# Optimization experiments

Measured on AMD Instinct MI355X. Metric: run time of the kernel, lower is better.

The kernel has to match this reference:

```python
import jax, jax.numpy as jnp
import numpy as np

NUM_HEADS = 8
MAX_REL = 32  # max_relative_positions
LN_EPS = 1e-5


def _conv1x1(x, W, b):
    # x: (B, C, H, W), W: (Cout, Cin), b: (Cout,)
    return jnp.einsum('bchw,oc->bohw', x, W) + b[None, :, None, None]


def setup_inputs() -> dict:
    key = jax.random.key(0)
    ks = jax.random.split(key, 10)
    B, C, H, W = 2, 512, 48, 48
    L = H * W
    s = 1.0 / np.sqrt(C)
    inp = {
        'x': jax.random.normal(ks[0], (B, C, H, W), jnp.float32),
        'mask': jax.random.randint(ks[1], (1, NUM_HEADS, L, L), 0, 2).astype(bool),
        'learnable_pos': jax.random.normal(ks[2], (1, C, H, W), jnp.float32) * 0.02,
        'Wq': jax.random.normal(ks[3], (C, C), jnp.float32) * s,
        'bq': jnp.zeros((C,), jnp.float32),
        'Wk': jax.random.normal(ks[4], (C, C), jnp.float32) * s,
        'bk': jnp.zeros((C,), jnp.float32),
        'Wv': jax.random.normal(ks[5], (C, C), jnp.float32) * s,
        'bv': jnp.zeros((C,), jnp.float32),
        'Wo': jax.random.normal(ks[6], (C, C), jnp.float32) * s,
        'bo': jnp.zeros((C,), jnp.float32),
        'rel_table': jax.random.normal(ks[7], (NUM_HEADS, 2 * MAX_REL + 1), jnp.float32) * 0.02,
        'ln_gamma': jnp.ones((C,), jnp.float32),
        'ln_beta': jnp.zeros((C,), jnp.float32),
    }
    return inp


def reference(x, mask, learnable_pos, Wq, bq, Wk, bk, Wv, bv, Wo, bo,
              rel_table, ln_gamma, ln_beta):
    B, C, H, W = x.shape
    L = H * W
    hd = C // NUM_HEADS
    residual = x

    xp = x + learnable_pos
    q = _conv1x1(xp, Wq, bq)
    k = _conv1x1(xp, Wk, bk)
    v = _conv1x1(xp, Wv, bv)

    def split_heads(t):  # (B,C,H,W) -> (B, heads, L, hd)
        return t.reshape(B, NUM_HEADS, hd, L).transpose(0, 1, 3, 2)

    q, k, v = split_heads(q), split_heads(k), split_heads(v)

    scale = 1.0 / np.sqrt(hd).astype(np.float32)
    scores = jnp.einsum('bhld,bhmd->bhlm', q, k) * scale  # (B,H,L,L)

    # relative positional bias per head
    pos = jnp.arange(L)
    rp = jnp.clip(pos[:, None] - pos[None, :], -MAX_REL, MAX_REL) + MAX_REL  # (L,L)
    scores = scores + rel_table[:, rp][None]  # (1,heads,L,L) broadcast

    scores = jnp.where(mask, scores, jnp.float32(-1e9))
    attn = jax.nn.softmax(scores, axis=-1)

    out = jnp.einsum('bhlm,bhmd->bhld', attn, v)  # (B,heads,L,hd)
    out = out.transpose(0, 1, 3, 2).reshape(B, C, H, W)
    out = _conv1x1(out, Wo, bo)

    y = residual + out
    # LayerNorm over channels (channels-last permute in original)
    yl = y.transpose(0, 2, 3, 1)  # (B,H,W,C)
    mu = jnp.mean(yl, axis=-1, keepdims=True)
    var = jnp.var(yl, axis=-1, keepdims=True)
    yl = (yl - mu) * jax.lax.rsqrt(var + LN_EPS) * ln_gamma + ln_beta
    return yl.transpose(0, 3, 1, 2)
```

## Files before the change

kernel.cpp:

```cpp
#include <hip/hip_runtime.h>
#include <cstdint>

#define L_SEQ 2304
#define CDIM  512
#define NHEADS 8
#define HD    64
#define LL    ((size_t)L_SEQ * L_SEQ)
#define ROWS_TOT (16 * L_SEQ)
#define PERBL ((size_t)2 * L_SEQ * 512)

typedef short  s8v  __attribute__((ext_vector_type(8)));
typedef float  f4v  __attribute__((ext_vector_type(4)));

__device__ __forceinline__ ushort f2bf(float f) {
    union { float f; uint32_t u; } v; v.f = f;
    uint32_t u = v.u;
    uint32_t r = (u + 0x7FFFu + ((u >> 16) & 1u)) >> 16;
    return (ushort)r;
}

__device__ __forceinline__ float bf2f(ushort u) {
    union { uint32_t u; float f; } v; v.u = (uint32_t)u << 16;
    return v.f;
}

__global__ __launch_bounds__(256) void prep(
    const float* __restrict__ Wq, const float* __restrict__ Wk,
    const float* __restrict__ Wv, const float* __restrict__ Wo,
    const float* __restrict__ x, const float* __restrict__ pos,
    ushort* __restrict__ wf, ushort* __restrict__ xt)
{
    __shared__ ushort T[64][72];
    const int bx = blockIdx.x;
    const int t  = threadIdx.x;
    if (bx < 512) {
        const int i    = bx * 256 + t;
        const int lane = i & 63;
        const int F    = (i >> 6) & 63;
        const int ob   = (i >> 12) & 7;
        const int mat  = i >> 15;
        const float* src = (mat == 0) ? Wq : (mat == 1) ? Wk : (mat == 2) ? Wv : Wo;
        const int row = ob * 64 + (F & 3) * 16 + (lane & 15);
        const int col = (F >> 2) * 32 + (lane >> 4) * 8;
        const float4 w0 = *(const float4*)&src[(size_t)row * 512 + col];
        const float4 w1 = *(const float4*)&src[(size_t)row * 512 + col + 4];
        ushort4 o0, o1;
        o0.x = f2bf(w0.x); o0.y = f2bf(w0.y); o0.z = f2bf(w0.z); o0.w = f2bf(w0.w);
        o1.x = f2bf(w1.x); o1.y = f2bf(w1.y); o1.z = f2bf(w1.z); o1.w = f2bf(w1.w);
        *(ushort4*)&wf[(size_t)i * 8]     = o0;
        *(ushort4*)&wf[(size_t)i * 8 + 4] = o1;
    } else {
        const int bb = bx - 512;
        const int l0 = (bb % 36) * 64;
        const int c0 = ((bb / 36) & 7) * 64;
        const int b  = bb / 288;
        const int cc = t >> 2;
        const int l4 = (t & 3) * 16;
        const size_t off  = ((size_t)b * CDIM + c0 + cc) * L_SEQ + l0 + l4;
        const size_t poff = (size_t)(c0 + cc) * L_SEQ + l0 + l4;
        #pragma unroll
        for (int j4 = 0; j4 < 4; j4++) {
            const float4 xv = *(const float4*)&x[off + j4 * 4];
            const float4 pv = *(const float4*)&pos[poff + j4 * 4];
            T[cc][l4 + j4 * 4 + 0] = f2bf(xv.x + pv.x);
            T[cc][l4 + j4 * 4 + 1] = f2bf(xv.y + pv.y);
            T[cc][l4 + j4 * 4 + 2] = f2bf(xv.z + pv.z);
            T[cc][l4 + j4 * 4 + 3] = f2bf(xv.w + pv.w);
        }
        __syncthreads();
        const int lr = t >> 2;
        const int c4 = (t & 3) * 16;
        ushort o[16];
        #pragma unroll
        for (int j = 0; j < 16; j++) o[j] = T[c4 + j][lr];
        ushort* dst = &xt[((size_t)b * L_SEQ + l0 + lr) * 512 + c0 + c4];
        *(ushort4*)&dst[0]  = *(ushort4*)&o[0];
        *(ushort4*)&dst[4]  = *(ushort4*)&o[4];
        *(ushort4*)&dst[8]  = *(ushort4*)&o[8];
        *(ushort4*)&dst[12] = *(ushort4*)&o[12];
    }
}

__global__ __launch_bounds__(256) void qkv_mfma(
    const ushort* __restrict__ xt, const ushort* __restrict__ wf,
    const float* __restrict__ bq, const float* __restrict__ bk,
    const float* __restrict__ bv,
    ushort* __restrict__ q_t, ushort* __restrict__ k_t, ushort* __restrict__ v_t)
{
    const int l0 = blockIdx.x * 64;
    const int ob = blockIdx.y;
    const int o0 = ob * 64;
    const int b  = blockIdx.z;
    const int t = threadIdx.x, w = t >> 6, lane = t & 63;
    const int n16 = lane & 15, q4 = lane >> 4;

    const ushort* A = xt + ((size_t)b * L_SEQ + l0 + w * 16 + n16) * 512 + q4 * 8;

    s8v areg[16];
    #pragma unroll
    for (int i = 0; i < 16; i++) areg[i] = *(const s8v*)&A[i * 32];

    const size_t lb = (size_t)lane * 8;

    f4v acc[3][4] = {};
    for (int ks = 0; ks < 16; ks++) {
        s8v bf[3][4];
        #pragma unroll
        for (int m = 0; m < 3; m++)
            #pragma unroll
            for (int t4 = 0; t4 < 4; t4++)
                bf[m][t4] = *(const s8v*)&wf[
                    ((size_t)((m * 8 + ob) * 64 + ks * 4 + t4)) * 512 + lb];
        const s8v a = areg[ks];
        #pragma unroll
        for (int m = 0; m < 3; m++)
            #pragma unroll
            for (int t4 = 0; t4 < 4; t4++)
                acc[m][t4] = __builtin_amdgcn_mfma_f32_16x16x32_bf16(a, bf[m][t4], acc[m][t4], 0, 0, 0);
    }

    const int h = ob;
    const int rowbase = l0 + w * 16 + q4 * 4;

    #pragma unroll
    for (int m = 0; m < 2; m++) {
        const float* bias = (m == 0) ? bq : bk;
        const float sc = (m == 0) ? 0.125f : 1.0f;
        ushort* op = (m == 0 ? q_t : k_t) + ((size_t)(b * NHEADS + h)) * L_SEQ * HD;
        #pragma unroll
        for (int t4 = 0; t4 < 4; t4++) {
            const float bi = bias[o0 + t4 * 16 + n16];
            #pragma unroll
            for (int r = 0; r < 4; r++)
                op[(size_t)(rowbase + r) * HD + t4 * 16 + n16] = f2bf((acc[m][t4][r] + bi) * sc);
        }
    }
    {
        ushort* op = v_t + ((size_t)(b * NHEADS + h)) * HD * L_SEQ;
        #pragma unroll
        for (int t4 = 0; t4 < 4; t4++) {
            const float bi = bv[o0 + t4 * 16 + n16];
            ushort4 st;
            st.x = f2bf(acc[2][t4][0] + bi);
            st.y = f2bf(acc[2][t4][1] + bi);
            st.z = f2bf(acc[2][t4][2] + bi);
            st.w = f2bf(acc[2][t4][3] + bi);
            *(ushort4*)&op[(size_t)(t4 * 16 + n16) * L_SEQ + rowbase] = st;
        }
    }
}

__global__ __launch_bounds__(256) void flash_attn_mfma(
    const ushort* __restrict__ q, const ushort* __restrict__ k,
    const ushort* __restrict__ vt, const int* __restrict__ mask,
    const float* __restrict__ rel_table, ushort* __restrict__ Opart,
    float* __restrict__ Lpart)
{
    __shared__ __align__(16) ushort Kf[2][512 * 8];
    __shared__ __align__(16) ushort Vf[2][512 * 8];
    __shared__ __align__(16) ushort Pb[4 * 16 * 72];
    __shared__ float rt[65];

    const int t    = threadIdx.x;
    const int id   = blockIdx.x;
    const int h    = id & 7;
    const int s2   = id >> 3;
    const int b    = s2 & 1;
    const int half = (s2 >> 1) & 1;
    const int qb   = s2 >> 2;
    const int bh   = b * NHEADS + h;
    const int l0   = qb * 64;
    const int w    = t >> 6;
    const int lane = t & 63;
    const int n16  = lane & 15;
    const int q4   = lane >> 4;

    if (t < 65) rt[t] = rel_table[h * 65 + t];

    const ushort* qp = q  + (size_t)bh * L_SEQ * HD;
    const ushort* kp = k  + (size_t)bh * L_SEQ * HD;
    const ushort* vp = vt + (size_t)bh * HD * L_SEQ;
    const int*    mp = mask + (size_t)h * LL;

    const int qrow = l0 + w * 16 + n16;
    const s8v qA0 = *(const s8v*)&qp[(size_t)qrow * HD + q4 * 8];
    const s8v qA1 = *(const s8v*)&qp[(size_t)qrow * HD + 32 + q4 * 8];

    f4v O[4] = {{0.f,0.f,0.f,0.f},{0.f,0.f,0.f,0.f},{0.f,0.f,0.f,0.f},{0.f,0.f,0.f,0.f}};
    float lrun[4] = {0.f, 0.f, 0.f, 0.f};

    int sKey[2], sD0[2], sDd[2];
    #pragma unroll
    for (int cc = 0; cc < 2; cc++) {
        const int c = t + cc * 256;
        const int g = c >> 6;
        const int sT = g >> 1, sS = g & 1;
        const int sQ = (c >> 4) & 3, sN = c & 15;
        sKey[cc] = sT * 16 + sN;
        sD0[cc]  = sS * 32 + sQ * 8;
        sDd[cc]  = sT * 16 + sN;
    }

    const int rowbase = l0 + w * 16 + q4 * 4;
    const int kbase = half * 1152;

    s8v kreg[2], vreg[2];
    int mreg[4][4];
    #pragma unroll
    for (int cc = 0; cc < 2; cc++) {
        kreg[cc] = *(const s8v*)&kp[(size_t)(kbase + sKey[cc]) * HD + sD0[cc]];
        vreg[cc] = *(const s8v*)&vp[(size_t)sDd[cc] * L_SEQ + kbase + sD0[cc]];
    }
    #pragma unroll
    for (int t4 = 0; t4 < 4; t4++)
        #pragma unroll
        for (int r = 0; r < 4; r++)
            mreg[t4][r] = mp[(size_t)(rowbase + r) * L_SEQ + kbase + t4 * 16 + n16];

    int par = 0;
    for (int mt = 0; mt < 18; mt++) {
        const int mb = kbase + mt * 64;
        ushort* Kb = &Kf[par][0];
        ushort* Vb = &Vf[par][0];
        #pragma unroll
        for (int cc = 0; cc < 2; cc++) {
            const int c = t + cc * 256;
            *(s8v*)&Kb[c * 8] = kreg[cc];
            *(s8v*)&Vb[c * 8] = vreg[cc];
        }
        __syncthreads();

        const int mb2 = (mt < 17) ? mb + 64 : mb;
        s8v knx[2], vnx[2];
        int mnx[4][4];
        #pragma unroll
        for (int cc = 0; cc < 2; cc++) {
            knx[cc] = *(const s8v*)&kp[(size_t)(mb2 + sKey[cc]) * HD + sD0[cc]];
            vnx[cc] = *(const s8v*)&vp[(size_t)sDd[cc] * L_SEQ + mb2 + sD0[cc]];
        }
        #pragma unroll
        for (int t4 = 0; t4 < 4; t4++)
            #pragma unroll
            for (int r = 0; r < 4; r++)
                mnx[t4][r] = mp[(size_t)(rowbase + r) * L_SEQ + mb2 + t4 * 16 + n16];

        f4v S[4];
        #pragma unroll
        for (int t4 = 0; t4 < 4; t4++) {
            const s8v b0 = *(const s8v*)&Kb[((t4 * 2 + 0) * 64 + lane) * 8];
            const s8v b1 = *(const s8v*)&Kb[((t4 * 2 + 1) * 64 + lane) * 8];
            f4v acc = {0.f, 0.f, 0.f, 0.f};
            acc = __builtin_amdgcn_mfma_f32_16x16x32_bf16(qA0, b0, acc, 0, 0, 0);
            acc = __builtin_amdgcn_mfma_f32_16x16x32_bf16(qA1, b1, acc, 0, 0, 0);
            S[t4] = acc;
        }

        #pragma unroll
        for (int t4 = 0; t4 < 4; t4++) {
            const int A = (l0 + w * 16) - (mb + t4 * 16);
            if (A >= 47) {
                const float bu = rt[64];
                #pragma unroll
                for (int r = 0; r < 4; r++) S[t4][r] += bu;
            } else if (A <= -47) {
                const float bu = rt[0];
                #pragma unroll
                for (int r = 0; r < 4; r++) S[t4][r] += bu;
            } else {
                #pragma unroll
                for (int r = 0; r < 4; r++) {
                    int dix = A + q4 * 4 + r - n16;
                    dix = min(max(dix, -32), 32) + 32;
                    S[t4][r] += rt[dix];
                }
            }
            #pragma unroll
            for (int r = 0; r < 4; r++)
                if (mreg[t4][r] == 0) S[t4][r] = -1e9f;
        }

        float sum[4] = {0.f, 0.f, 0.f, 0.f};
        #pragma unroll
        for (int r = 0; r < 4; r++) {
            #pragma unroll
            for (int t4 = 0; t4 < 4; t4++) {
                const float p = __expf(S[t4][r]);
                sum[r] += p;
                Pb[w * 1152 + (q4 * 4 + r) * 72 + t4 * 16 + n16] = f2bf(p);
            }
        }

        const s8v pf0 = *(const s8v*)&Pb[w * 1152 + n16 * 72 + q4 * 8];
        const s8v pf1 = *(const s8v*)&Pb[w * 1152 + n16 * 72 + 32 + q4 * 8];
        #pragma unroll
        for (int t4 = 0; t4 < 4; t4++) {
            f4v o = O[t4];
            const s8v v0 = *(const s8v*)&Vb[((t4 * 2 + 0) * 64 + lane) * 8];
            const s8v v1 = *(const s8v*)&Vb[((t4 * 2 + 1) * 64 + lane) * 8];
            o = __builtin_amdgcn_mfma_f32_16x16x32_bf16(pf0, v0, o, 0, 0, 0);
            o = __builtin_amdgcn_mfma_f32_16x16x32_bf16(pf1, v1, o, 0, 0, 0);
            O[t4] = o;
        }

        #pragma unroll
        for (int r = 0; r < 4; r++) {
            float s = sum[r];
            s += __shfl_xor(s, 1);
            s += __shfl_xor(s, 2);
            s += __shfl_xor(s, 4);
            s += __shfl_xor(s, 8);
            lrun[r] += s;
        }

        #pragma unroll
        for (int cc = 0; cc < 2; cc++) { kreg[cc] = knx[cc]; vreg[cc] = vnx[cc]; }
        #pragma unroll
        for (int t4 = 0; t4 < 4; t4++)
            #pragma unroll
            for (int r = 0; r < 4; r++)
                mreg[t4][r] = mnx[t4][r];
        par ^= 1;
    }

    ushort* op = Opart + (size_t)half * PERBL + (size_t)b * L_SEQ * 512;
    #pragma unroll
    for (int r = 0; r < 4; r++) {
        const size_t base = (size_t)(rowbase + r) * 512 + h * 64;
        #pragma unroll
        for (int t4 = 0; t4 < 4; t4++)
            op[base + t4 * 16 + n16] = f2bf(O[t4][r]);
    }
    if (n16 == 0) {
        const size_t sb = (size_t)half * ROWS_TOT + (size_t)bh * L_SEQ;
        #pragma unroll
        for (int r = 0; r < 4; r++)
            Lpart[sb + rowbase + r] = lrun[r];
    }
}

__global__ __launch_bounds__(256) void out_mfma(
    const ushort* __restrict__ Opart, const float* __restrict__ Lp,
    const ushort* __restrict__ wf, const float* __restrict__ bo,
    const float* __restrict__ x, float* __restrict__ y)
{
    const int l0 = blockIdx.x * 64;
    const int ob = blockIdx.y;
    const int o0 = ob * 64;
    const int b  = blockIdx.z;
    const int t = threadIdx.x, w = t >> 6, lane = t & 63;
    const int n16 = lane & 15, q4 = lane >> 4;

    const int l = l0 + w * 16 + n16;

    float fsc[8];
    #pragma unroll
    for (int h = 0; h < 8; h++) {
        const size_t s = (size_t)(b * NHEADS + h) * L_SEQ + l;
        fsc[h] = 1.0f / (Lp[s] + Lp[ROWS_TOT + s]);
    }

    const ushort* o0p = Opart + ((size_t)b * L_SEQ + l) * 512 + q4 * 8;
    const ushort* o1p = o0p + PERBL;

    s8v areg[16];
    #pragma unroll
    for (int ks = 0; ks < 16; ks++) {
        const ushort4 a0 = *(const ushort4*)&o0p[ks * 32];
        const ushort4 a1 = *(const ushort4*)&o0p[ks * 32 + 4];
        const ushort4 c0 = *(const ushort4*)&o1p[ks * 32];
        const ushort4 c1 = *(const ushort4*)&o1p[ks * 32 + 4];
        const float f = fsc[ks >> 1];
        s8v a;
        a[0] = (short)f2bf((bf2f(a0.x) + bf2f(c0.x)) * f);
        a[1] = (short)f2bf((bf2f(a0.y) + bf2f(c0.y)) * f);
        a[2] = (short)f2bf((bf2f(a0.z) + bf2f(c0.z)) * f);
        a[3] = (short)f2bf((bf2f(a0.w) + bf2f(c0.w)) * f);
        a[4] = (short)f2bf((bf2f(a1.x) + bf2f(c1.x)) * f);
        a[5] = (short)f2bf((bf2f(a1.y) + bf2f(c1.y)) * f);
        a[6] = (short)f2bf((bf2f(a1.z) + bf2f(c1.z)) * f);
        a[7] = (short)f2bf((bf2f(a1.w) + bf2f(c1.w)) * f);
        areg[ks] = a;
    }

    const size_t lb = (size_t)lane * 8;

    f4v acc[4] = {{0.f,0.f,0.f,0.f},{0.f,0.f,0.f,0.f},{0.f,0.f,0.f,0.f},{0.f,0.f,0.f,0.f}};
    for (int ks = 0; ks < 16; ks++) {
        s8v bf[4];
        #pragma unroll
        for (int t4 = 0; t4 < 4; t4++)
            bf[t4] = *(const s8v*)&wf[
                ((size_t)((3 * 8 + ob) * 64 + ks * 4 + t4)) * 512 + lb];
        const s8v a = areg[ks];
        #pragma unroll
        for (int t4 = 0; t4 < 4; t4++)
            acc[t4] = __builtin_amdgcn_mfma_f32_16x16x32_bf16(a, bf[t4], acc[t4], 0, 0, 0);
    }

    const int rowbase = l0 + w * 16 + q4 * 4;
    #pragma unroll
    for (int t4 = 0; t4 < 4; t4++) {
        const int o = o0 + t4 * 16 + n16;
        const float bi = bo[o];
        const size_t off = ((size_t)b * CDIM + o) * L_SEQ + rowbase;
        const float4 xv = *(const float4*)&x[off];
        float4 st;
        st.x = acc[t4][0] + bi + xv.x;
        st.y = acc[t4][1] + bi + xv.y;
        st.z = acc[t4][2] + bi + xv.z;
        st.w = acc[t4][3] + bi + xv.w;
        *(float4*)&y[off] = st;
    }
}

__global__ __launch_bounds__(256) void ln_kernel(
    float* __restrict__ y, const float* __restrict__ gamma,
    const float* __restrict__ beta)
{
    const int t = threadIdx.x;
    const int p = t & 31;
    const int g = t >> 5;
    const int pos = blockIdx.x * 32 + p;
    const int b = (pos >= L_SEQ) ? 1 : 0;
    const int l = pos - b * L_SEQ;
    float* col = y + (size_t)b * CDIM * L_SEQ + l;

    float s = 0.f, sq = 0.f;
    for (int c = g * 64; c < g * 64 + 64; c++) {
        const float v = col[(size_t)c * L_SEQ];
        s += v; sq += v * v;
    }
    __shared__ float S1[8][32];
    __shared__ float S2[8][32];
    S1[g][p] = s; S2[g][p] = sq;
    __syncthreads();
    if (t < 32) {
        float ss = 0.f, qq = 0.f;
        #pragma unroll
        for (int gg = 0; gg < 8; gg++) { ss += S1[gg][t]; qq += S2[gg][t]; }
        const float mu = ss * (1.0f / CDIM);
        const float var = qq * (1.0f / CDIM) - mu * mu;
        S1[0][t] = mu;
        S2[0][t] = rsqrtf(var + 1e-5f);
    }
    __syncthreads();
    const float mu = S1[0][p];
    const float rs = S2[0][p];
    for (int c = g * 64; c < g * 64 + 64; c++) {
        const float v = col[(size_t)c * L_SEQ];
        col[(size_t)c * L_SEQ] = (v - mu) * rs * gamma[c] + beta[c];
    }
}

extern "C" void kernel_launch(void* const* d_in, const int* in_sizes, int n_in,
                              void* d_out, int out_size, void* d_ws, size_t ws_size,
                              hipStream_t stream) {
    const float* x    = (const float*)d_in[0];
    const int* mask   = (const int*)d_in[1];
    const float* pos  = (const float*)d_in[2];
    const float* Wq   = (const float*)d_in[3];
    const float* bq   = (const float*)d_in[4];
    const float* Wk   = (const float*)d_in[5];
    const float* bk   = (const float*)d_in[6];
    const float* Wv   = (const float*)d_in[7];
    const float* bv   = (const float*)d_in[8];
    const float* Wo   = (const float*)d_in[9];
    const float* bo   = (const float*)d_in[10];
    const float* rel  = (const float*)d_in[11];
    const float* gam  = (const float*)d_in[12];
    const float* bet  = (const float*)d_in[13];

    ushort* qw  = (ushort*)d_ws;
    ushort* kw  = qw + PERBL;
    ushort* vw  = kw + PERBL;
    ushort* xtw = vw + PERBL;
    ushort* wbw = xtw + PERBL;
    ushort* Opart = wbw + (size_t)4 * 262144;
    float* Lpart = (float*)(Opart + 2 * PERBL);
    float* y = (float*)d_out;

    prep<<<dim3(512 + 576), 256, 0, stream>>>(Wq, Wk, Wv, Wo, x, pos, wbw, xtw);

    qkv_mfma<<<dim3(L_SEQ / 64, CDIM / 64, 2), 256, 0, stream>>>(
        xtw, wbw, bq, bk, bv, qw, kw, vw);

    flash_attn_mfma<<<dim3(1152), 256, 0, stream>>>(qw, kw, vw, mask, rel,
                                                    Opart, Lpart);

    out_mfma<<<dim3(L_SEQ / 64, CDIM / 64, 2), 256, 0, stream>>>(
        Opart, Lpart, wbw, bo, x, y);

    ln_kernel<<<(2 * L_SEQ) / 32, 256, 0, stream>>>(y, gam, bet);
}
```

Measured before the change: 366.0 us.

## Split attention keys four ways and QKV projection per matrix for more blocks

The flash attention kernel now splits each query block's keys into four 576-key chunks instead of two, doubling the grid. The output projection sums four partial outputs and denominators. The QKV projection launches one block per matrix (Q, K or V) rather than computing all three per block, tripling that grid and cutting accumulators. The attention K/V shared buffers go from double to single buffering with an extra barrier, which lowers LDS use but serialises the store and compute phases. The extra partials add workspace traffic and reduction work in out_mfma.

```diff
diff --git a/kernel.cpp b/kernel.cpp
--- a/kernel.cpp
+++ b/kernel.cpp
@@ -87,10 +87,11 @@
     const float* __restrict__ bv,
     ushort* __restrict__ q_t, ushort* __restrict__ k_t, ushort* __restrict__ v_t)
 {
-    const int l0 = blockIdx.x * 64;
-    const int ob = blockIdx.y;
-    const int o0 = ob * 64;
-    const int b  = blockIdx.z;
+    const int l0  = blockIdx.x * 64;
+    const int ob  = blockIdx.y;
+    const int o0  = ob * 64;
+    const int mat = blockIdx.z % 3;
+    const int b   = blockIdx.z / 3;
     const int t = threadIdx.x, w = t >> 6, lane = t & 63;
     const int n16 = lane & 15, q4 = lane >> 4;
 
@@ -101,50 +102,44 @@
     for (int i = 0; i < 16; i++) areg[i] = *(const s8v*)&A[i * 32];
 
     const size_t lb = (size_t)lane * 8;
-
-    f4v acc[3][4] = {};
+    const size_t wbase = (size_t)(mat * 8 + ob) * 64;
+
+    f4v acc[4] = {{0.f,0.f,0.f,0.f},{0.f,0.f,0.f,0.f},{0.f,0.f,0.f,0.f},{0.f,0.f,0.f,0.f}};
     for (int ks = 0; ks < 16; ks++) {
-        s8v bf[3][4];
-        #pragma unroll
-        for (int m = 0; m < 3; m++)
-            #pragma unroll
-            for (int t4 = 0; t4 < 4; t4++)
-                bf[m][t4] = *(const s8v*)&wf[
-                    ((size_t)((m * 8 + ob) * 64 + ks * 4 + t4)) * 512 + lb];
+        s8v bf[4];
+        #pragma unroll
+        for (int t4 = 0; t4 < 4; t4++)
+            bf[t4] = *(const s8v*)&wf[(wbase + ks * 4 + t4) * 512 + lb];
         const s8v a = areg[ks];
         #pragma unroll
-        for (int m = 0; m < 3; m++)
-            #pragma unroll
-            for (int t4 = 0; t4 < 4; t4++)
-                acc[m][t4] = __builtin_amdgcn_mfma_f32_16x16x32_bf16(a, bf[m][t4], acc[m][t4], 0, 0, 0);
+        for (int t4 = 0; t4 < 4; t4++)
+            acc[t4] = __builtin_amdgcn_mfma_f32_16x16x32_bf16(a, bf[t4], acc[t4], 0, 0, 0);
     }
 
     const int h = ob;
     const int rowbase = l0 + w * 16 + q4 * 4;
 
-    #pragma unroll
-    for (int m = 0; m < 2; m++) {
-        const float* bias = (m == 0) ? bq : bk;
-        const float sc = (m == 0) ? 0.125f : 1.0f;
-        ushort* op = (m == 0 ? q_t : k_t) + ((size_t)(b * NHEADS + h)) * L_SEQ * HD;
+    if (mat < 2) {
+        const float* bias = (mat == 0) ? bq : bk;
+        const float sc = (mat == 0) ? 0.125f : 1.0f;
+        ushort* op = (mat == 0 ? q_t : k_t) + ((size_t)(b * NHEADS + h)) * L_SEQ * HD;
         #pragma unroll
         for (int t4 = 0; t4 < 4; t4++) {
             const float bi = bias[o0 + t4 * 16 + n16];
             #pragma unroll
             for (int r = 0; r < 4; r++)
-                op[(size_t)(rowbase + r) * HD + t4 * 16 + n16] = f2bf((acc[m][t4][r] + bi) * sc);
-        }
-    }
-    {
+                op[(size_t)(rowbase + r) * HD + t4 * 16 + n16] = f2bf((acc[t4][r] + bi) * sc);
+        }
+    } else {
         ushort* op = v_t + ((size_t)(b * NHEADS + h)) * HD * L_SEQ;
         #pragma unroll
         for (int t4 = 0; t4 < 4; t4++) {
             const float bi = bv[o0 + t4 * 16 + n16];
             ushort4 st;
-            st.x = f2bf(acc[2][t4][0] + bi);
-            st.y = f2bf(acc[2][t4][1] + bi);
-            st.z = f2bf(acc[2][t4][2] + bi);
-            st.w = f2bf(acc[2][t4][3] + bi);
+            st.x = f2bf(acc[t4][0] + bi);
+            st.y = f2bf(acc[t4][1] + bi);
+            st.z = f2bf(acc[t4][2] + bi);
+            st.w = f2bf(acc[t4][3] + bi);
             *(ushort4*)&op[(size_t)(t4 * 16 + n16) * L_SEQ + rowbase] = st;
         }
     }
@@ -156,8 +151,8 @@
     const float* __restrict__ rel_table, ushort* __restrict__ Opart,
     float* __restrict__ Lpart)
 {
-    __shared__ __align__(16) ushort Kf[2][512 * 8];
-    __shared__ __align__(16) ushort Vf[2][512 * 8];
+    __shared__ __align__(16) ushort Kf[512 * 8];
+    __shared__ __align__(16) ushort Vf[512 * 8];
     __shared__ __align__(16) ushort Pb[4 * 16 * 72];
     __shared__ float rt[65];
 
@@ -166,8 +161,8 @@
     const int h    = id & 7;
     const int s2   = id >> 3;
     const int b    = s2 & 1;
-    const int half = (s2 >> 1) & 1;
-    const int qb   = s2 >> 2;
+    const int half = (s2 >> 1) & 3;
+    const int qb   = s2 >> 3;
     const int bh   = b * NHEADS + h;
     const int l0   = qb * 64;
     const int w    = t >> 6;
@@ -202,7 +197,7 @@
     }
 
     const int rowbase = l0 + w * 16 + q4 * 4;
-    const int kbase = half * 1152;
+    const int kbase = half * 576;
 
     s8v kreg[2], vreg[2];
     int mreg[4][4];
@@ -217,20 +212,18 @@
         for (int r = 0; r < 4; r++)
             mreg[t4][r] = mp[(size_t)(rowbase + r) * L_SEQ + kbase + t4 * 16 + n16];
 
-    int par = 0;
-    for (int mt = 0; mt < 18; mt++) {
+    for (int mt = 0; mt < 9; mt++) {
         const int mb = kbase + mt * 64;
-        ushort* Kb = &Kf[par][0];
-        ushort* Vb = &Vf[par][0];
+        __syncthreads();
         #pragma unroll
         for (int cc = 0; cc < 2; cc++) {
             const int c = t + cc * 256;
-            *(s8v*)&Kb[c * 8] = kreg[cc];
-            *(s8v*)&Vb[c * 8] = vreg[cc];
+            *(s8v*)&Kf[c * 8] = kreg[cc];
+            *(s8v*)&Vf[c * 8] = vreg[cc];
         }
         __syncthreads();
 
-        const int mb2 = (mt < 17) ? mb + 64 : mb;
+        const int mb2 = (mt < 8) ? mb + 64 : mb;
         s8v knx[2], vnx[2];
         int mnx[4][4];
         #pragma unroll
@@ -247,8 +240,8 @@
         f4v S[4];
         #pragma unroll
         for (int t4 = 0; t4 < 4; t4++) {
-            const s8v b0 = *(const s8v*)&Kb[((t4 * 2 + 0) * 64 + lane) * 8];
-            const s8v b1 = *(const s8v*)&Kb[((t4 * 2 + 1) * 64 + lane) * 8];
+            const s8v b0 = *(const s8v*)&Kf[((t4 * 2 + 0) * 64 + lane) * 8];
+            const s8v b1 = *(const s8v*)&Kf[((t4 * 2 + 1) * 64 + lane) * 8];
             f4v acc = {0.f, 0.f, 0.f, 0.f};
             acc = __builtin_amdgcn_mfma_f32_16x16x32_bf16(qA0, b0, acc, 0, 0, 0);
             acc = __builtin_amdgcn_mfma_f32_16x16x32_bf16(qA1, b1, acc, 0, 0, 0);
@@ -295,8 +288,8 @@
         #pragma unroll
         for (int t4 = 0; t4 < 4; t4++) {
             f4v o = O[t4];
-            const s8v v0 = *(const s8v*)&Vb[((t4 * 2 + 0) * 64 + lane) * 8];
-            const s8v v1 = *(const s8v*)&Vb[((t4 * 2 + 1) * 64 + lane) * 8];
+            const s8v v0 = *(const s8v*)&Vf[((t4 * 2 + 0) * 64 + lane) * 8];
+            const s8v v1 = *(const s8v*)&Vf[((t4 * 2 + 1) * 64 + lane) * 8];
             o = __builtin_amdgcn_mfma_f32_16x16x32_bf16(pf0, v0, o, 0, 0, 0);
             o = __builtin_amdgcn_mfma_f32_16x16x32_bf16(pf1, v1, o, 0, 0, 0);
             O[t4] = o;
@@ -319,7 +312,6 @@
             #pragma unroll
             for (int r = 0; r < 4; r++)
                 mreg[t4][r] = mnx[t4][r];
-        par ^= 1;
     }
 
     ushort* op = Opart + (size_t)half * PERBL + (size_t)b * L_SEQ * 512;
@@ -356,29 +348,31 @@
     #pragma unroll
     for (int h = 0; h < 8; h++) {
         const size_t s = (size_t)(b * NHEADS + h) * L_SEQ + l;
-        fsc[h] = 1.0f / (Lp[s] + Lp[ROWS_TOT + s]);
+        fsc[h] = 1.0f / (Lp[s] + Lp[ROWS_TOT + s] +
+                         Lp[2 * (size_t)ROWS_TOT + s] + Lp[3 * (size_t)ROWS_TOT + s]);
     }
 
     const ushort* o0p = Opart + ((size_t)b * L_SEQ + l) * 512 + q4 * 8;
-    const ushort* o1p = o0p + PERBL;
 
     s8v areg[16];
     #pragma unroll
     for (int ks = 0; ks < 16; ks++) {
-        const ushort4 a0 = *(const ushort4*)&o0p[ks * 32];
-        const ushort4 a1 = *(const ushort4*)&o0p[ks * 32 + 4];
-        const ushort4 c0 = *(const ushort4*)&o1p[ks * 32];
-        const ushort4 c1 = *(const ushort4*)&o1p[ks * 32 + 4];
         const float f = fsc[ks >> 1];
+        float v[8];
+        #pragma unroll
+        for (int j = 0; j < 8; j++) v[j] = 0.f;
+        #pragma unroll
+        for (int pq = 0; pq < 4; pq++) {
+            const ushort4 a0 = *(const ushort4*)&o0p[(size_t)pq * PERBL + ks * 32];
+            const ushort4 a1 = *(const ushort4*)&o0p[(size_t)pq * PERBL + ks * 32 + 4];
+            v[0] += bf2f(a0.x); v[1] += bf2f(a0.y);
+            v[2] += bf2f(a0.z); v[3] += bf2f(a0.w);
+            v[4] += bf2f(a1.x); v[5] += bf2f(a1.y);
+            v[6] += bf2f(a1.z); v[7] += bf2f(a1.w);
+        }
         s8v a;
-        a[0] = (short)f2bf((bf2f(a0.x) + bf2f(c0.x)) * f);
-        a[1] = (short)f2bf((bf2f(a0.y) + bf2f(c0.y)) * f);
-        a[2] = (short)f2bf((bf2f(a0.z) + bf2f(c0.z)) * f);
-        a[3] = (short)f2bf((bf2f(a0.w) + bf2f(c0.w)) * f);
-        a[4] = (short)f2bf((bf2f(a1.x) + bf2f(c1.x)) * f);
-        a[5] = (short)f2bf((bf2f(a1.y) + bf2f(c1.y)) * f);
-        a[6] = (short)f2bf((bf2f(a1.z) + bf2f(c1.z)) * f);
-        a[7] = (short)f2bf((bf2f(a1.w) + bf2f(c1.w)) * f);
+        #pragma unroll
+        for (int j = 0; j < 8; j++) a[j] = (short)f2bf(v[j] * f);
         areg[ks] = a;
     }
 
@@ -476,15 +470,15 @@
     ushort* xtw = vw + PERBL;
     ushort* wbw = xtw + PERBL;
     ushort* Opart = wbw + (size_t)4 * 262144;
-    float* Lpart = (float*)(Opart + 2 * PERBL);
+    float* Lpart = (float*)(Opart + 4 * PERBL);
     float* y = (float*)d_out;
 
     prep<<<dim3(512 + 576), 256, 0, stream>>>(Wq, Wk, Wv, Wo, x, pos, wbw, xtw);
 
-    qkv_mfma<<<dim3(L_SEQ / 64, CDIM / 64, 2), 256, 0, stream>>>(
+    qkv_mfma<<<dim3(L_SEQ / 64, CDIM / 64, 6), 256, 0, stream>>>(
         xtw, wbw, bq, bk, bv, qw, kw, vw);
 
-    flash_attn_mfma<<<dim3(1152), 256, 0, stream>>>(qw, kw, vw, mask, rel,
+    flash_attn_mfma<<<dim3(2304), 256, 0, stream>>>(qw, kw, vw, mask, rel,
                                                     Opart, Lpart);
 
     out_mfma<<<dim3(L_SEQ / 64, CDIM / 64, 2), 256, 0, stream>>>(
```

Measured after the change: 376.2 us. 1.03x slower.
